# Kernel optimization log

Measured on AMD Instinct MI355X. Metric: run time of the kernel, lower is better.

Reference implementation:

```python
import jax, jax.numpy as jnp
import numpy as np

K = 1_000_000      # number of sparse (2D-det, 3D-anchor) candidate pairs
ROWS = 200         # max 2D detections
COLS = 70400       # number of 3D anchors (200*176*2)
SENTINEL = -9999999.0


def setup_inputs() -> dict:
    key = jax.random.key(0)
    ks = jax.random.split(key, 12)
    input_1 = jax.random.normal(ks[0], (1, 4, 1, K), dtype=jnp.float32)
    idx0 = jax.random.randint(ks[1], (K,), 0, ROWS)
    idx1 = jax.random.randint(ks[2], (K,), 0, COLS)
    tensor_index = jnp.stack([idx0, idx1], axis=1).astype(jnp.int64)
    # fuse_2d_3d: 1x1 Conv2d stack 4->18->36->36->1 (weights as (out,in) matrices)
    def w(k, o, i):
        return jax.random.normal(k, (o, i), dtype=jnp.float32) * (1.0 / np.sqrt(i))
    return {
        "input_1": input_1,
        "tensor_index": tensor_index,
        "W1": w(ks[3], 18, 4),  "b1": jnp.zeros((18,), jnp.float32),
        "W2": w(ks[4], 36, 18), "b2": jnp.zeros((36,), jnp.float32),
        "W3": w(ks[5], 36, 36), "b3": jnp.zeros((36,), jnp.float32),
        "W4": w(ks[6], 1, 36),  "b4": jnp.zeros((1,), jnp.float32),
    }


def reference(input_1, tensor_index, W1, b1, W2, b2, W3, b3, W4, b4):
    # 1x1 convs over (1,4,1,K) are channel matmuls over the K pair axis.
    x = input_1[0, :, 0, :]                                   # (4, K)
    h = jax.nn.relu(jnp.dot(W1, x) + b1[:, None])             # (18, K)
    h = jax.nn.relu(jnp.dot(W2, h) + b2[:, None])             # (36, K)
    h = jax.nn.relu(jnp.dot(W3, h) + b3[:, None])             # (36, K)
    v = (jnp.dot(W4, h) + b4[:, None])[0]                     # (K,) fused score per pair
    # Scatter into dense sentinel-filled grid, then max-reduce the 200 dim
    # (equivalent to MaxPool2d([200,1]) in the original).
    dense = jnp.full((ROWS, COLS), SENTINEL, dtype=input_1.dtype)
    dense = dense.at[tensor_index[:, 0], tensor_index[:, 1]].max(v)
    out = jnp.max(dense, axis=0).reshape(1, -1, 1)            # (1, 70400, 1)
    flag = 1
    return (out, flag)
```

## Files before the change

### kernel.cpp

```cpp
#include <hip/hip_runtime.h>

#define KN 1000000
#define NCOLS 70400
#define NTHR 256
#define CHUNK 1024
#define KBLK 977
#define NBUK 275
#define CAP 24

typedef _Float16 f16x4 __attribute__((ext_vector_type(4)));
typedef float    f32x4 __attribute__((ext_vector_type(4)));

#define MFMA16(a, b, c) __builtin_amdgcn_mfma_f32_16x16x16f16((a), (b), (c), 0, 0, 0)

__device__ __forceinline__ unsigned encodeF(float f) {
    unsigned b = __float_as_uint(f);
    return (b & 0x80000000u) ? ~b : (b | 0x80000000u);
}
__device__ __forceinline__ float decodeF(unsigned e) {
    unsigned b = (e & 0x80000000u) ? (e & 0x7fffffffu) : ~e;
    return __uint_as_float(b);
}
#define ENC_SENT 0x34E76980u

#define OW1 0
#define OB1 72
#define OW2 90
#define OB2 738
#define OW3 774
#define OB3 2070
#define OW4 2106
#define OB4 2142
#define NWTS 2143


__device__ uint2    g_bin[(size_t)NBUK * KBLK * CAP];
__device__ unsigned g_cnt[NBUK * KBLK];

__global__ __launch_bounds__(NTHR)
void mlp_bin(const float* __restrict__ x, const int* __restrict__ tidx,
             const float* __restrict__ W1, const float* __restrict__ b1,
             const float* __restrict__ W2, const float* __restrict__ b2,
             const float* __restrict__ W3, const float* __restrict__ b3,
             const float* __restrict__ W4, const float* __restrict__ b4)
{
    __shared__ float    sw[NWTS];
    __shared__ unsigned bcnt[NBUK];

    const int t    = threadIdx.x;
    const int lane = t & 63;
    const int quad = lane >> 4;
    const int n    = lane & 15;

    for (int i = t; i < 72;   i += NTHR) sw[OW1 + i] = W1[i];
    for (int i = t; i < 18;   i += NTHR) sw[OB1 + i] = b1[i];
    for (int i = t; i < 648;  i += NTHR) sw[OW2 + i] = W2[i];
    for (int i = t; i < 36;   i += NTHR) sw[OB2 + i] = b2[i];
    for (int i = t; i < 1296; i += NTHR) sw[OW3 + i] = W3[i];
    for (int i = t; i < 36;   i += NTHR) sw[OB3 + i] = b3[i];
    for (int i = t; i < 36;   i += NTHR) sw[OW4 + i] = W4[i];
    if (t == 0) sw[OB4] = b4[0];
    for (int i = t; i < NBUK; i += NTHR) bcnt[i] = 0u;
    __syncthreads();

    auto af = [&](int off, int OUT, int IN, int tt, int s) {
        f16x4 r;
#pragma unroll
        for (int j = 0; j < 4; ++j) {
            const int m = tt * 16 + n;
            const int k = s * 16 + quad * 4 + j;
            const float w = (m < OUT && k < IN) ? sw[off + m * IN + k] : 0.0f;
            r[j] = (_Float16)w;
        }
        return r;
    };
    auto bv = [&](int off, int OUT, int tt) {
        f32x4 c;
#pragma unroll
        for (int r = 0; r < 4; ++r) {
            const int m = tt * 16 + quad * 4 + r;
            c[r] = (m < OUT) ? sw[off + m] : 0.0f;
        }
        return c;
    };

    const f16x4 A1_0  = af(OW1, 18,  4, 0, 0), A1_1  = af(OW1, 18,  4, 1, 0);
    const f16x4 A2_00 = af(OW2, 36, 18, 0, 0), A2_01 = af(OW2, 36, 18, 0, 1);
    const f16x4 A2_10 = af(OW2, 36, 18, 1, 0), A2_11 = af(OW2, 36, 18, 1, 1);
    const f16x4 A2_20 = af(OW2, 36, 18, 2, 0), A2_21 = af(OW2, 36, 18, 2, 1);
    const f16x4 A3_00 = af(OW3, 36, 36, 0, 0), A3_01 = af(OW3, 36, 36, 0, 1), A3_02 = af(OW3, 36, 36, 0, 2);
    const f16x4 A3_10 = af(OW3, 36, 36, 1, 0), A3_11 = af(OW3, 36, 36, 1, 1), A3_12 = af(OW3, 36, 36, 1, 2);
    const f16x4 A3_20 = af(OW3, 36, 36, 2, 0), A3_21 = af(OW3, 36, 36, 2, 1), A3_22 = af(OW3, 36, 36, 2, 2);

    const f32x4 C1_0 = bv(OB1, 18, 0), C1_1 = bv(OB1, 18, 1);
    const f32x4 C2_0 = bv(OB2, 36, 0), C2_1 = bv(OB2, 36, 1), C2_2 = bv(OB2, 36, 2);
    const f32x4 C3_0 = bv(OB3, 36, 0), C3_1 = bv(OB3, 36, 1), C3_2 = bv(OB3, 36, 2);
    const f32x4 V4_0 = bv(OW4, 36, 0), V4_1 = bv(OW4, 36, 1), V4_2 = bv(OW4, 36, 2);
    const float b4s  = sw[OB4];

    const int base = blockIdx.x * CHUNK;
    const int lim  = (base + CHUNK < KN) ? base + CHUNK : KN;

    auto rl = [](f32x4 v) {
        f16x4 h;
#pragma unroll
        for (int r = 0; r < 4; ++r) h[r] = (_Float16)fmaxf(v[r], 0.0f);
        return h;
    };

    int kb = base + (t >> 6) * 32;
    float cxa0, cxa1, cxa2, cxa3, cxb0, cxb1, cxb2, cxb3;
    int cca = 0, ccb = 0;
    if (kb < lim) {
        cxa0 = x[0 * KN + kb + n];      cxb0 = x[0 * KN + kb + 16 + n];
        cxa1 = x[1 * KN + kb + n];      cxb1 = x[1 * KN + kb + 16 + n];
        cxa2 = x[2 * KN + kb + n];      cxb2 = x[2 * KN + kb + 16 + n];
        cxa3 = x[3 * KN + kb + n];      cxb3 = x[3 * KN + kb + 16 + n];
        cca  = tidx[2 * (kb + n) + 1];  ccb  = tidx[2 * (kb + 16 + n) + 1];
    }

    for (; kb < lim; kb += 128) {
        const int kbn = kb + 128;
        const float xa0 = cxa0, xa1 = cxa1, xa2 = cxa2, xa3 = cxa3;
        const float xb0 = cxb0, xb1 = cxb1, xb2 = cxb2, xb3 = cxb3;
        const int cola = cca, colb = ccb;
        if (kbn < lim) {
            cxa0 = x[0 * KN + kbn + n];      cxb0 = x[0 * KN + kbn + 16 + n];
            cxa1 = x[1 * KN + kbn + n];      cxb1 = x[1 * KN + kbn + 16 + n];
            cxa2 = x[2 * KN + kbn + n];      cxb2 = x[2 * KN + kbn + 16 + n];
            cxa3 = x[3 * KN + kbn + n];      cxb3 = x[3 * KN + kbn + 16 + n];
            cca  = tidx[2 * (kbn + n) + 1];  ccb  = tidx[2 * (kbn + 16 + n) + 1];
        }

        f16x4 B0a = {}, B0b = {};
        if (quad == 0) {
            B0a[0] = (_Float16)xa0; B0a[1] = (_Float16)xa1;
            B0a[2] = (_Float16)xa2; B0a[3] = (_Float16)xa3;
            B0b[0] = (_Float16)xb0; B0b[1] = (_Float16)xb1;
            B0b[2] = (_Float16)xb2; B0b[3] = (_Float16)xb3;
        }

        f32x4 d1a0 = MFMA16(A1_0, B0a, C1_0);
        f32x4 d1b0 = MFMA16(A1_0, B0b, C1_0);
        f32x4 d1a1 = MFMA16(A1_1, B0a, C1_1);
        f32x4 d1b1 = MFMA16(A1_1, B0b, C1_1);
        const f16x4 B1a0 = rl(d1a0), B1a1 = rl(d1a1);
        const f16x4 B1b0 = rl(d1b0), B1b1 = rl(d1b1);

        f32x4 d2a0 = MFMA16(A2_00, B1a0, C2_0);  d2a0 = MFMA16(A2_01, B1a1, d2a0);
        f32x4 d2b0 = MFMA16(A2_00, B1b0, C2_0);  d2b0 = MFMA16(A2_01, B1b1, d2b0);
        f32x4 d2a1 = MFMA16(A2_10, B1a0, C2_1);  d2a1 = MFMA16(A2_11, B1a1, d2a1);
        f32x4 d2b1 = MFMA16(A2_10, B1b0, C2_1);  d2b1 = MFMA16(A2_11, B1b1, d2b1);
        f32x4 d2a2 = MFMA16(A2_20, B1a0, C2_2);  d2a2 = MFMA16(A2_21, B1a1, d2a2);
        f32x4 d2b2 = MFMA16(A2_20, B1b0, C2_2);  d2b2 = MFMA16(A2_21, B1b1, d2b2);
        const f16x4 B2a0 = rl(d2a0), B2a1 = rl(d2a1), B2a2 = rl(d2a2);
        const f16x4 B2b0 = rl(d2b0), B2b1 = rl(d2b1), B2b2 = rl(d2b2);

        f32x4 d3a0 = MFMA16(A3_00, B2a0, C3_0);
        d3a0 = MFMA16(A3_01, B2a1, d3a0);  d3a0 = MFMA16(A3_02, B2a2, d3a0);
        f32x4 d3b0 = MFMA16(A3_00, B2b0, C3_0);
        d3b0 = MFMA16(A3_01, B2b1, d3b0);  d3b0 = MFMA16(A3_02, B2b2, d3b0);
        f32x4 d3a1 = MFMA16(A3_10, B2a0, C3_1);
        d3a1 = MFMA16(A3_11, B2a1, d3a1);  d3a1 = MFMA16(A3_12, B2a2, d3a1);
        f32x4 d3b1 = MFMA16(A3_10, B2b0, C3_1);
        d3b1 = MFMA16(A3_11, B2b1, d3b1);  d3b1 = MFMA16(A3_12, B2b2, d3b1);
        f32x4 d3a2 = MFMA16(A3_20, B2a0, C3_2);
        d3a2 = MFMA16(A3_21, B2a1, d3a2);  d3a2 = MFMA16(A3_22, B2a2, d3a2);
        f32x4 d3b2 = MFMA16(A3_20, B2b0, C3_2);
        d3b2 = MFMA16(A3_21, B2b1, d3b2);  d3b2 = MFMA16(A3_22, B2b2, d3b2);

        float pa = 0.0f, pb = 0.0f;
#pragma unroll
        for (int r = 0; r < 4; ++r) {
            pa = fmaf(V4_0[r], fmaxf(d3a0[r], 0.0f), pa);
            pa = fmaf(V4_1[r], fmaxf(d3a1[r], 0.0f), pa);
            pa = fmaf(V4_2[r], fmaxf(d3a2[r], 0.0f), pa);
            pb = fmaf(V4_0[r], fmaxf(d3b0[r], 0.0f), pb);
            pb = fmaf(V4_1[r], fmaxf(d3b1[r], 0.0f), pb);
            pb = fmaf(V4_2[r], fmaxf(d3b2[r], 0.0f), pb);
        }
        pa += __shfl_xor(pa, 16);  pa += __shfl_xor(pa, 32);
        pb += __shfl_xor(pb, 16);  pb += __shfl_xor(pb, 32);

        if (quad < 2) {
            const int   col = (quad == 0) ? cola : colb;
            const float pv  = (quad == 0) ? pa   : pb;
            const unsigned enc = encodeF(pv + b4s) - ENC_SENT;
            const int bk = col >> 8;
            const unsigned slot = atomicAdd(&bcnt[bk], 1u);
            if (slot < CAP) {
                uint2 e;
                e.x = (unsigned)(col & 255);
                e.y = enc;
                g_bin[((size_t)bk * KBLK + blockIdx.x) * CAP + slot] = e;
            }
        }
    }

    __syncthreads();
    for (int i = t; i < NBUK; i += NTHR) {
        unsigned c = bcnt[i];
        g_cnt[i * KBLK + blockIdx.x] = (c > CAP) ? CAP : c;
    }
}

__global__ __launch_bounds__(NTHR)
void bucket_reduce(float* __restrict__ out, int out_size)
{
    __shared__ unsigned tab[256];
    const int b = blockIdx.x;
    const int t = threadIdx.x;

    tab[t] = 0u;
    __syncthreads();

    for (int rb = t; rb < KBLK; rb += NTHR) {
        unsigned c = g_cnt[b * KBLK + rb];
        if (c > CAP) c = CAP;
        const uint2* reg = &g_bin[((size_t)b * KBLK + rb) * CAP];
        for (unsigned s = 0; s < c; ++s) {
            const uint2 e = reg[s];
            atomicMax(&tab[e.x], e.y);
        }
    }
    __syncthreads();

    const int gid = b * 256 + t;
    if (gid < out_size) out[gid] = decodeF(tab[t] + ENC_SENT);
    if (b == 0) {
        for (int i = NCOLS + t; i < out_size; i += NTHR) out[i] = 1.0f;
    }
}

extern "C" void kernel_launch(void* const* d_in, const int* in_sizes, int n_in,
                              void* d_out, int out_size, void* d_ws, size_t ws_size,
                              hipStream_t stream) {
    const float* x    = (const float*)d_in[0];
    const int*   tidx = (const int*)d_in[1];
    const float* W1 = (const float*)d_in[2];
    const float* b1 = (const float*)d_in[3];
    const float* W2 = (const float*)d_in[4];
    const float* b2 = (const float*)d_in[5];
    const float* W3 = (const float*)d_in[6];
    const float* b3 = (const float*)d_in[7];
    const float* W4 = (const float*)d_in[8];
    const float* b4 = (const float*)d_in[9];

    mlp_bin<<<KBLK, NTHR, 0, stream>>>(x, tidx, W1, b1, W2, b2, W3, b3, W4, b4);

    bucket_reduce<<<NBUK, NTHR, 0, stream>>>((float*)d_out, out_size);
}
```

Baseline: 141.0 us.

## Replace per-block bucket binning with linear log plus range-partitioned shared-memory reduction

The MLP kernel now writes every (column, encoded score) pair into a flat global log instead of per-block capped buckets. A second kernel scans log slices per column range, reduces with shared-memory atomicMax, and stores per-slice partial tables. A third kernel merges the 64 partials per column and decodes. This removes the bucket capacity limit and the serial per-thread bucket loops, at the cost of rereading the log once per range and writing and reading large partial tables.

```diff
diff --git a/kernel.cpp b/kernel.cpp
--- a/kernel.cpp
+++ b/kernel.cpp
@@ -5,8 +5,10 @@
 #define NTHR 256
 #define CHUNK 1024
 #define KBLK 977
-#define NBUK 275
-#define CAP 24
+#define RANGE 8800
+#define NRANGE 8
+#define B2 64
+#define SLICE 15625
 
 typedef _Float16 f16x4 __attribute__((ext_vector_type(4)));
 typedef float    f32x4 __attribute__((ext_vector_type(4)));
@@ -34,18 +36,17 @@
 #define NWTS 2143
 
 
-__device__ uint2    g_bin[(size_t)NBUK * KBLK * CAP];
-__device__ unsigned g_cnt[NBUK * KBLK];
+__device__ uint2    g_log[KN];
+__device__ unsigned g_tab[(size_t)NRANGE * B2 * RANGE];
 
 __global__ __launch_bounds__(NTHR)
-void mlp_bin(const float* __restrict__ x, const int* __restrict__ tidx,
+void mlp_log(const float* __restrict__ x, const int* __restrict__ tidx,
              const float* __restrict__ W1, const float* __restrict__ b1,
              const float* __restrict__ W2, const float* __restrict__ b2,
              const float* __restrict__ W3, const float* __restrict__ b3,
              const float* __restrict__ W4, const float* __restrict__ b4)
 {
-    __shared__ float    sw[NWTS];
-    __shared__ unsigned bcnt[NBUK];
+    __shared__ float sw[NWTS];
 
     const int t    = threadIdx.x;
     const int lane = t & 63;
@@ -60,7 +61,6 @@
     for (int i = t; i < 36;   i += NTHR) sw[OB3 + i] = b3[i];
     for (int i = t; i < 36;   i += NTHR) sw[OW4 + i] = W4[i];
     if (t == 0) sw[OB4] = b4[0];
-    for (int i = t; i < NBUK; i += NTHR) bcnt[i] = 0u;
     __syncthreads();
 
     auto af = [&](int off, int OUT, int IN, int tt, int s) {
@@ -182,54 +182,62 @@
         pa += __shfl_xor(pa, 16);  pa += __shfl_xor(pa, 32);
         pb += __shfl_xor(pb, 16);  pb += __shfl_xor(pb, 32);
 
-        if (quad < 2) {
-            const int   col = (quad == 0) ? cola : colb;
-            const float pv  = (quad == 0) ? pa   : pb;
-            const unsigned enc = encodeF(pv + b4s) - ENC_SENT;
-            const int bk = col >> 8;
-            const unsigned slot = atomicAdd(&bcnt[bk], 1u);
-            if (slot < CAP) {
-                uint2 e;
-                e.x = (unsigned)(col & 255);
-                e.y = enc;
-                g_bin[((size_t)bk * KBLK + blockIdx.x) * CAP + slot] = e;
-            }
-        }
-    }
-
+        if (lane < 32) {
+            const int   col = (lane < 16) ? cola : colb;
+            const float pv  = (lane < 16) ? pa   : pb;
+            uint2 e;
+            e.x = (unsigned)col;
+            e.y = encodeF(pv + b4s) - ENC_SENT;
+            g_log[kb + lane] = e;
+        }
+
+        kb = kb;
+    }
+}
+
+__global__ __launch_bounds__(NTHR)
+void range_reduce()
+{
+    __shared__ unsigned tab[RANGE];
+    const int rangeId = blockIdx.x >> 6;
+    const int s       = blockIdx.x & (B2 - 1);
+    const int t       = threadIdx.x;
+    const unsigned cbase = (unsigned)(rangeId * RANGE);
+
+    for (int i = t; i < RANGE; i += NTHR) tab[i] = 0u;
     __syncthreads();
-    for (int i = t; i < NBUK; i += NTHR) {
-        unsigned c = bcnt[i];
-        g_cnt[i * KBLK + blockIdx.x] = (c > CAP) ? CAP : c;
-    }
+
+    const uint2* lg = g_log + (size_t)s * SLICE;
+    for (int i = t; i < SLICE; i += NTHR) {
+        const uint2 e = lg[i];
+        const unsigned c = e.x - cbase;
+        if (c < RANGE) atomicMax(&tab[c], e.y);
+    }
+    __syncthreads();
+
+    unsigned* dstT = g_tab + ((size_t)rangeId * B2 + s) * RANGE;
+    for (int i = t; i < RANGE; i += NTHR) dstT[i] = tab[i];
 }
 
 __global__ __launch_bounds__(NTHR)
-void bucket_reduce(float* __restrict__ out, int out_size)
+void merge_decode(float* __restrict__ out, int out_size)
 {
-    __shared__ unsigned tab[256];
-    const int b = blockIdx.x;
-    const int t = threadIdx.x;
-
-    tab[t] = 0u;
-    __syncthreads();
-
-    for (int rb = t; rb < KBLK; rb += NTHR) {
-        unsigned c = g_cnt[b * KBLK + rb];
-        if (c > CAP) c = CAP;
-        const uint2* reg = &g_bin[((size_t)b * KBLK + rb) * CAP];
-        for (unsigned s = 0; s < c; ++s) {
-            const uint2 e = reg[s];
-            atomicMax(&tab[e.x], e.y);
-        }
-    }
-    __syncthreads();
-
-    const int gid = b * 256 + t;
-    if (gid < out_size) out[gid] = decodeF(tab[t] + ENC_SENT);
-    if (b == 0) {
-        for (int i = NCOLS + t; i < out_size; i += NTHR) out[i] = 1.0f;
-    }
+    const int gid = blockIdx.x * NTHR + threadIdx.x;
+    if (gid >= out_size) return;
+    float r = 1.0f;
+    if (gid < NCOLS) {
+        const int rangeId = gid / RANGE;
+        const int c       = gid - rangeId * RANGE;
+        const unsigned* tp = g_tab + (size_t)rangeId * B2 * RANGE + c;
+        unsigned m = 0u;
+#pragma unroll 8
+        for (int s = 0; s < B2; ++s) {
+            const unsigned v = tp[(size_t)s * RANGE];
+            m = (v > m) ? v : m;
+        }
+        r = decodeF(m + ENC_SENT);
+    }
+    out[gid] = r;
 }
 
 extern "C" void kernel_launch(void* const* d_in, const int* in_sizes, int n_in,
@@ -246,7 +254,10 @@
     const float* W4 = (const float*)d_in[8];
     const float* b4 = (const float*)d_in[9];
 
-    mlp_bin<<<KBLK, NTHR, 0, stream>>>(x, tidx, W1, b1, W2, b2, W3, b3, W4, b4);
-
-    bucket_reduce<<<NBUK, NTHR, 0, stream>>>((float*)d_out, out_size);
-}
+    mlp_log<<<KBLK, NTHR, 0, stream>>>(x, tidx, W1, b1, W2, b2, W3, b3, W4, b4);
+
+    range_reduce<<<NRANGE * B2, NTHR, 0, stream>>>();
+
+    merge_decode<<<(out_size + NTHR - 1) / NTHR, NTHR, 0, stream>>>(
+        (float*)d_out, out_size);
+}
```

Result: no change. 142.0 us (+0.7%).
